# Kernel optimization log

Hardware: AMD Instinct MI355X
Metric: run time of the kernel (lower is better)

The kernel has to match this reference:

```python
import jax, jax.numpy as jnp
import numpy as np

B, C, H, W, N = 2, 128, 800, 640, 8192


def bilinear_sample(img, grid):
    """torch.F.grid_sample, mode='bilinear', padding_mode='border', align_corners=True.
    img: (B, C, H, W); grid: (B, P, 2) with (x, y) in [-1, 1]. Returns (B, C, P)."""
    _, _, h, w = img.shape
    x = jnp.clip((grid[..., 0] + 1.0) * 0.5 * (w - 1), 0.0, w - 1)  # border clip
    y = jnp.clip((grid[..., 1] + 1.0) * 0.5 * (h - 1), 0.0, h - 1)
    x0 = jnp.floor(x); y0 = jnp.floor(y)
    x0i = x0.astype(jnp.int32); y0i = y0.astype(jnp.int32)
    x1i = jnp.minimum(x0i + 1, w - 1); y1i = jnp.minimum(y0i + 1, h - 1)
    wx = (x - x0)[:, None, :]; wy = (y - y0)[:, None, :]
    g = jax.vmap(lambda im, yi, xi: im[:, yi, xi])  # per-batch gather -> (C, P)
    v00 = g(img, y0i, x0i); v01 = g(img, y0i, x1i)
    v10 = g(img, y1i, x0i); v11 = g(img, y1i, x1i)
    return (v00 * (1 - wx) * (1 - wy) + v01 * wx * (1 - wy)
            + v10 * (1 - wx) * wy + v11 * wx * wy)


def setup_inputs() -> dict:
    key = jax.random.key(0)
    ks = jax.random.split(key, 12)
    img = jax.random.normal(ks[0], (B, C, H, W), jnp.float32)
    verts = jax.random.uniform(ks[1], (B, N, 2), jnp.float32, minval=-1.0, maxval=1.0)
    # shift_delta Conv1d(C, 18, k=1) -- original inits to 0; use small random to exercise gathers
    W_sd = jax.random.normal(ks[2], (18, C), jnp.float32) * 0.01
    b_sd = jnp.zeros((18,), jnp.float32)
    s1 = 1.0 / np.sqrt(C + 2); s2 = 1.0 / np.sqrt(C)
    W_d1 = jax.random.normal(ks[3], (C, C + 2), jnp.float32) * s1
    b_d1 = jax.random.normal(ks[4], (C,), jnp.float32) * 0.01
    W_d2 = jax.random.normal(ks[5], (C, C), jnp.float32) * s2
    b_d2 = jax.random.normal(ks[6], (C,), jnp.float32) * 0.01
    # sum_neighbourhood Conv2d(C, C, kernel (1, 9)) -> weight (C, C, 9) after squeezing kh=1
    W_sn = jax.random.normal(ks[7], (C, C, 9), jnp.float32) * np.sqrt(2.0 / (C * 9))
    b_sn = jnp.zeros((C,), jnp.float32)
    W_c1 = jax.random.normal(ks[8], (C, C + 2), jnp.float32) * s1
    b_c1 = jax.random.normal(ks[9], (C,), jnp.float32) * 0.01
    W_c2 = jax.random.normal(ks[10], (C, C), jnp.float32) * s2
    b_c2 = jax.random.normal(ks[11], (C,), jnp.float32) * 0.01
    return dict(image_features=img, vertices=verts, W_sd=W_sd, b_sd=b_sd,
                W_d1=W_d1, b_d1=b_d1, W_d2=W_d2, b_d2=b_d2,
                W_sn=W_sn, b_sn=b_sn, W_c1=W_c1, b_c1=b_c1, W_c2=W_c2, b_c2=b_c2)


def reference(image_features, vertices, W_sd, b_sd, W_d1, b_d1, W_d2, b_d2,
              W_sn, b_sn, W_c1, b_c1, W_c2, b_c2):
    b, n, _ = vertices.shape
    c = image_features.shape[1]
    # sample at vertex centers: (B, C, N)
    feat_c = bilinear_sample(image_features, vertices)
    # Conv1d k=1 -> per-vertex linear producing 9 learned 2D offsets
    sd = (jnp.einsum('oc,bcn->bno', W_sd, feat_c) + b_sd).reshape(b, n, 9, 2)
    sd = sd.at[:, :, 0, :].set(0.0)  # offset 0 is the center itself
    nb = vertices[:, :, None, :] + sd                         # (B, N, 9, 2)
    f = bilinear_sample(image_features, nb.reshape(b, n * 9, 2)).reshape(b, c, n, 9)
    f = jnp.concatenate([f, nb.transpose(0, 3, 1, 2)], axis=1)  # (B, C+2, N, 9)
    d = f - f[:, :, :, :1]                                    # diff from center
    d = d.transpose(0, 3, 2, 1)                               # (B, 9, N, C+2)
    d = d @ W_d1.T + b_d1
    d = d @ W_d2.T + b_d2                                     # (B, 9, N, C)
    # Conv2d kernel (1, 9): contract neighbourhood axis -> (B, N, C)
    d = jnp.einsum('bknc,ock->bno', d, W_sn) + b_sn
    center = f[:, :, :, 0].transpose(0, 2, 1)                 # (B, N, C+2)
    center = (center @ W_c1.T + b_c1) @ W_c2.T + b_c2
    return center + d
```

## Files before the change

### kernel.cpp

```cpp
#include <hip/hip_runtime.h>
#include <cstdint>

#define BB 2
#define CC 128
#define IH 800
#define IW 640
#define NN 8192
#define HWp (IH * IW)
#define CE 130
#define WSL (CE * CC)
#define VPB 16

#define FADDR(e, v) (((e) << 4) + ((((e) >> 2)) << 2) + (v))
#define FSZ (FADDR(129, 15) + 1)


__device__ __forceinline__ void coords(float gx, float gy, int& xs, int& ys,
                                       float& ax, float& ay) {
  float x = (gx + 1.0f) * 0.5f * (float)(IW - 1);
  x = fminf(fmaxf(x, 0.0f), (float)(IW - 1));
  float y = (gy + 1.0f) * 0.5f * (float)(IH - 1);
  y = fminf(fmaxf(y, 0.0f), (float)(IH - 1));
  xs = min((int)x, IW - 2);
  ys = min((int)y, IH - 2);
  ax = x - (float)xs;
  ay = y - (float)ys;
}

struct GatIssue {
  float4 v0, v1;
  float ax, ay;
};

__device__ __forceinline__ GatIssue gat_issue(const float* __restrict__ imgT,
                                              int b, float gx, float gy, int l) {
  int xs, ys; float ax, ay;
  coords(gx, gy, xs, ys, ax, ay);
  const float* base = imgT + ((size_t)b * HWp + (size_t)ys * IW + xs) * CC;
  GatIssue g;
  g.v0 = *(const float4*)(base + l * 4);
  g.v1 = *(const float4*)(base + (size_t)IW * CC + l * 4);
  g.ax = ax; g.ay = ay;
  return g;
}

__device__ __forceinline__ float4 gat_finish(const GatIssue& g, int l) {
  float my = 1.0f - g.ay, mx = 1.0f - g.ax;
  float4 vy;
  vy.x = g.v0.x * my + g.v1.x * g.ay;
  vy.y = g.v0.y * my + g.v1.y * g.ay;
  vy.z = g.v0.z * my + g.v1.z * g.ay;
  vy.w = g.v0.w * my + g.v1.w * g.ay;
  float4 vo;
  vo.x = __shfl_xor(vy.x, 32, 64);
  vo.y = __shfl_xor(vy.y, 32, 64);
  vo.z = __shfl_xor(vy.z, 32, 64);
  vo.w = __shfl_xor(vy.w, 32, 64);
  float4 r;
  if (l < 32) {
    r.x = vy.x * mx + vo.x * g.ax;
    r.y = vy.y * mx + vo.y * g.ax;
    r.z = vy.z * mx + vo.z * g.ax;
    r.w = vy.w * mx + vo.w * g.ax;
  } else {
    r.x = vo.x * mx + vy.x * g.ax;
    r.y = vo.y * mx + vy.y * g.ax;
    r.z = vo.z * mx + vy.z * g.ax;
    r.w = vo.w * mx + vy.w * g.ax;
  }
  return r;
}

__device__ __forceinline__ float gat1_chw(const float* __restrict__ img, int b,
                                          int c, int xs, int ys, float ax, float ay) {
  const float* p = img + ((size_t)(b * CC + c) * IH + ys) * IW + xs;
  float v00 = p[0], v01 = p[1], v10 = p[IW], v11 = p[IW + 1];
  float my = 1.0f - ay, mx = 1.0f - ax;
  return (v00 * mx + v01 * ax) * my + (v10 * mx + v11 * ax) * ay;
}


__global__ void prep1(const float* __restrict__ W_d1, const float* __restrict__ b_d1,
                      const float* __restrict__ W_d2, const float* __restrict__ b_d2,
                      const float* __restrict__ W_c1, const float* __restrict__ b_c1,
                      const float* __restrict__ W_c2, const float* __restrict__ b_c2,
                      float* __restrict__ Wd, float* __restrict__ bdf,
                      float* __restrict__ Wcc, float* __restrict__ bcc) {
  int id = blockIdx.x;
  int e = threadIdx.x;
  if (id < 128) {
    int c = id;
    float acc = 0.0f;
    for (int c2 = 0; c2 < 128; ++c2)
      acc = fmaf(W_d2[c * 128 + c2], W_d1[c2 * CE + e], acc);
    Wd[c * CE + e] = acc;
    if (e == 0) {
      float bb = b_d2[c];
      for (int c2 = 0; c2 < 128; ++c2) bb = fmaf(W_d2[c * 128 + c2], b_d1[c2], bb);
      bdf[c] = bb;
    }
  } else {
    int o = id - 128;
    float acc = 0.0f;
    for (int c2 = 0; c2 < 128; ++c2)
      acc = fmaf(W_c2[o * 128 + c2], W_c1[c2 * CE + e], acc);
    Wcc[o * CE + e] = acc;
    if (e == 0) {
      float bb = b_c2[o];
      for (int c2 = 0; c2 < 128; ++c2) bb = fmaf(W_c2[o * 128 + c2], b_c1[c2], bb);
      bcc[o] = bb;
    }
  }
}

__global__ void prep2(const float* __restrict__ W_sn, const float* __restrict__ b_sn,
                      const float* __restrict__ Wd, const float* __restrict__ bdf,
                      const float* __restrict__ Wcc, const float* __restrict__ bcc,
                      float* __restrict__ Wcen, float* __restrict__ Wnb,
                      float* __restrict__ btot) {
  int eb = blockIdx.x;
  int o = threadIdx.x;
  float acc[9] = {0, 0, 0, 0, 0, 0, 0, 0, 0};
  float bacc = 0.0f;
  for (int c = 0; c < 128; ++c) {
    float wd = Wd[c * CE + eb];
    float bd = bdf[c];
    const float* sn = W_sn + (size_t)o * 1152 + c * 9;
    float ssum = 0.0f;
#pragma unroll
    for (int k = 0; k < 9; ++k) {
      float s = sn[k];
      acc[k] = fmaf(s, wd, acc[k]);
      ssum += s;
    }
    bacc = fmaf(ssum, bd, bacc);
  }
  float sum18 = 0.0f;
#pragma unroll
  for (int k = 1; k < 9; ++k) {
    Wnb[(size_t)(k - 1) * WSL + eb * 128 + o] = acc[k];
    sum18 += acc[k];
  }
  Wcen[eb * 128 + o] = Wcc[o * CE + eb] - sum18;
  if (eb == 0) btot[o] = bcc[o] + bacc + b_sn[o];
}


__global__ __launch_bounds__(256) void transpose_k(const float* __restrict__ img,
                                                   float* __restrict__ imgT) {
  __shared__ float tile[128][69];
  int b = blockIdx.y;
  size_t p0 = (size_t)blockIdx.x * 64;
  int t = threadIdx.x;
  int pq = t & 15, cr = t >> 4;
  float4 vr[8];
#pragma unroll
  for (int i = 0; i < 8; ++i) {
    int c = cr + (i << 4);
    vr[i] = *(const float4*)(img + (size_t)(b * CC + c) * HWp + p0 + pq * 4);
  }
#pragma unroll
  for (int i = 0; i < 8; ++i) {
    int c = cr + (i << 4);
    tile[c][pq * 4 + 0] = vr[i].x;
    tile[c][pq * 4 + 1] = vr[i].y;
    tile[c][pq * 4 + 2] = vr[i].z;
    tile[c][pq * 4 + 3] = vr[i].w;
  }
  __syncthreads();
  int c4 = (t & 31) << 2, pw = t >> 5;
#pragma unroll
  for (int i = 0; i < 8; ++i) {
    int p = pw + (i << 3);
    float4 v;
    v.x = tile[c4 + 0][p];
    v.y = tile[c4 + 1][p];
    v.z = tile[c4 + 2][p];
    v.w = tile[c4 + 3][p];
    *(float4*)(imgT + ((size_t)b * HWp + p0 + p) * CC + c4) = v;
  }
}


template <bool HWC>
__global__ __launch_bounds__(256) void fused_all(
    const float* __restrict__ imgp, const float* __restrict__ verts,
    const float* __restrict__ W_sd, const float* __restrict__ b_sd,
    const float* __restrict__ Wcen, const float* __restrict__ Wnb,
    const float* __restrict__ btot, float* __restrict__ out) {
  __shared__ __align__(16) float f[FSZ];
  __shared__ float sdl[VPB][18];
  __shared__ float nbc[VPB][16];
  __shared__ float red[128][17];
  int t = threadIdx.x;
  int o = t & 127, hs = t >> 7;
  int e0 = hs * 65;
  int v0 = blockIdx.x * VPB;
  int wv = t >> 6, l = t & 63;
  float acc[VPB] = {};

  if constexpr (HWC) {
    GatIssue g[4];
    float gxy[4][2];
#pragma unroll
    for (int s = 0; s < 4; ++s) {
      int vid = v0 + wv * 4 + s, b = vid >> 13;
      float gx = verts[vid * 2], gy = verts[vid * 2 + 1];
      gxy[s][0] = gx; gxy[s][1] = gy;
      g[s] = gat_issue(imgp, b, gx, gy, l);
    }
#pragma unroll
    for (int s = 0; s < 4; ++s) {
      int v = wv * 4 + s;
      float4 r = gat_finish(g[s], l);
      if (l < 32) {
        f[FADDR(4 * l + 0, v)] = r.x;
        f[FADDR(4 * l + 1, v)] = r.y;
        f[FADDR(4 * l + 2, v)] = r.z;
        f[FADDR(4 * l + 3, v)] = r.w;
      }
      if (l == 32) { f[FADDR(128, v)] = gxy[s][0]; f[FADDR(129, v)] = gxy[s][1]; }
    }
  } else {
    for (int s = 0; s < 4; ++s) {
      int v = wv * 4 + s, vid = v0 + v, b = vid >> 13;
      float gx = verts[vid * 2], gy = verts[vid * 2 + 1];
      int xs, ys; float ax, ay;
      coords(gx, gy, xs, ys, ax, ay);
      f[FADDR(l, v)] = gat1_chw(imgp, b, l, xs, ys, ax, ay);
      f[FADDR(l + 64, v)] = gat1_chw(imgp, b, l + 64, xs, ys, ax, ay);
      if (l == 0) { f[FADDR(128, v)] = gx; f[FADDR(129, v)] = gy; }
    }
  }
  __syncthreads();

  for (int idx = t; idx < VPB * 18; idx += 256) {
    int v = idx / 18, oo = idx - v * 18;
    float a = b_sd[oo];
    for (int c = 0; c < 128; ++c)
      a = fmaf(W_sd[oo * 128 + c], f[FADDR(c, v)], a);
    sdl[v][oo] = a;
  }

  {
    const float* Ws = Wcen;
    for (int e = e0; e < e0 + 65; ++e) {
      float w = Ws[e * 128 + o];
      const float4* fp = (const float4*)&f[FADDR(e, 0)];
      float4 fa = fp[0], fb = fp[1], fc = fp[2], fd = fp[3];
      acc[0]  = fmaf(fa.x, w, acc[0]);  acc[1]  = fmaf(fa.y, w, acc[1]);
      acc[2]  = fmaf(fa.z, w, acc[2]);  acc[3]  = fmaf(fa.w, w, acc[3]);
      acc[4]  = fmaf(fb.x, w, acc[4]);  acc[5]  = fmaf(fb.y, w, acc[5]);
      acc[6]  = fmaf(fb.z, w, acc[6]);  acc[7]  = fmaf(fb.w, w, acc[7]);
      acc[8]  = fmaf(fc.x, w, acc[8]);  acc[9]  = fmaf(fc.y, w, acc[9]);
      acc[10] = fmaf(fc.z, w, acc[10]); acc[11] = fmaf(fc.w, w, acc[11]);
      acc[12] = fmaf(fd.x, w, acc[12]); acc[13] = fmaf(fd.y, w, acc[13]);
      acc[14] = fmaf(fd.z, w, acc[14]); acc[15] = fmaf(fd.w, w, acc[15]);
    }
  }
  __syncthreads();

  {
    int v = t >> 4, j = t & 15, k = (j >> 1) + 1, comp = j & 1;
    int vid = v0 + v;
    nbc[v][j] = verts[vid * 2 + comp] + sdl[v][k * 2 + comp];
  }
  __syncthreads();

  for (int k = 0; k < 8; ++k) {
    if constexpr (HWC) {
      GatIssue g[4];
      float gxy[4][2];
#pragma unroll
      for (int s = 0; s < 4; ++s) {
        int v = wv * 4 + s, vid = v0 + v, b = vid >> 13;
        float gx = nbc[v][k * 2], gy = nbc[v][k * 2 + 1];
        gxy[s][0] = gx; gxy[s][1] = gy;
        g[s] = gat_issue(imgp, b, gx, gy, l);
      }
#pragma unroll
      for (int s = 0; s < 4; ++s) {
        int v = wv * 4 + s;
        float4 r = gat_finish(g[s], l);
        if (l < 32) {
          f[FADDR(4 * l + 0, v)] = r.x;
          f[FADDR(4 * l + 1, v)] = r.y;
          f[FADDR(4 * l + 2, v)] = r.z;
          f[FADDR(4 * l + 3, v)] = r.w;
        }
        if (l == 32) { f[FADDR(128, v)] = gxy[s][0]; f[FADDR(129, v)] = gxy[s][1]; }
      }
    } else {
      for (int s = 0; s < 4; ++s) {
        int v = wv * 4 + s, vid = v0 + v, b = vid >> 13;
        float gx = nbc[v][k * 2], gy = nbc[v][k * 2 + 1];
        int xs, ys; float ax, ay;
        coords(gx, gy, xs, ys, ax, ay);
        f[FADDR(l, v)] = gat1_chw(imgp, b, l, xs, ys, ax, ay);
        f[FADDR(l + 64, v)] = gat1_chw(imgp, b, l + 64, xs, ys, ax, ay);
        if (l == 0) { f[FADDR(128, v)] = gx; f[FADDR(129, v)] = gy; }
      }
    }
    __syncthreads();
    const float* Ws = Wnb + (size_t)k * WSL;
    for (int e = e0; e < e0 + 65; ++e) {
      float w = Ws[e * 128 + o];
      const float4* fp = (const float4*)&f[FADDR(e, 0)];
      float4 fa = fp[0], fb = fp[1], fc = fp[2], fd = fp[3];
      acc[0]  = fmaf(fa.x, w, acc[0]);  acc[1]  = fmaf(fa.y, w, acc[1]);
      acc[2]  = fmaf(fa.z, w, acc[2]);  acc[3]  = fmaf(fa.w, w, acc[3]);
      acc[4]  = fmaf(fb.x, w, acc[4]);  acc[5]  = fmaf(fb.y, w, acc[5]);
      acc[6]  = fmaf(fb.z, w, acc[6]);  acc[7]  = fmaf(fb.w, w, acc[7]);
      acc[8]  = fmaf(fc.x, w, acc[8]);  acc[9]  = fmaf(fc.y, w, acc[9]);
      acc[10] = fmaf(fc.z, w, acc[10]); acc[11] = fmaf(fc.w, w, acc[11]);
      acc[12] = fmaf(fd.x, w, acc[12]); acc[13] = fmaf(fd.y, w, acc[13]);
      acc[14] = fmaf(fd.z, w, acc[14]); acc[15] = fmaf(fd.w, w, acc[15]);
    }
    __syncthreads();
  }

  if (hs) {
#pragma unroll
    for (int j = 0; j < VPB; ++j) red[o][j] = acc[j];
  }
  __syncthreads();
  if (!hs) {
    float bt = btot[o];
#pragma unroll
    for (int j = 0; j < VPB; ++j)
      out[(size_t)(v0 + j) * CC + o] = acc[j] + red[o][j] + bt;
  }
}


extern "C" void kernel_launch(void* const* d_in, const int* in_sizes, int n_in,
                              void* d_out, int out_size, void* d_ws, size_t ws_size,
                              hipStream_t stream) {
  const float* img   = (const float*)d_in[0];
  const float* verts = (const float*)d_in[1];
  const float* W_sd  = (const float*)d_in[2];
  const float* b_sd  = (const float*)d_in[3];
  const float* W_d1  = (const float*)d_in[4];
  const float* b_d1  = (const float*)d_in[5];
  const float* W_d2  = (const float*)d_in[6];
  const float* b_d2  = (const float*)d_in[7];
  const float* W_sn  = (const float*)d_in[8];
  const float* b_sn  = (const float*)d_in[9];
  const float* W_c1  = (const float*)d_in[10];
  const float* b_c1  = (const float*)d_in[11];
  const float* W_c2  = (const float*)d_in[12];
  const float* b_c2  = (const float*)d_in[13];
  float* out = (float*)d_out;
  float* ws = (float*)d_ws;

  const size_t imgT_fl = (size_t)BB * HWp * CC;
  const size_t wt_fl   = 11 * (size_t)WSL + 384;
  bool hwc = ws_size >= (imgT_fl + wt_fl) * sizeof(float);

  float* base = ws;
  float* imgT = nullptr;
  if (hwc) { imgT = ws; base = ws + imgT_fl; }
  float* Wd   = base;  base += WSL;
  float* bdf  = base;  base += 128;
  float* Wcc  = base;  base += WSL;
  float* bcc  = base;  base += 128;
  float* Wcen = base;  base += WSL;
  float* Wnb  = base;  base += 8 * WSL;
  float* btot = base;

  if (hwc) transpose_k<<<dim3(HWp / 64, BB), 256, 0, stream>>>(img, imgT);
  prep1<<<256, 130, 0, stream>>>(W_d1, b_d1, W_d2, b_d2, W_c1, b_c1, W_c2, b_c2,
                                 Wd, bdf, Wcc, bcc);
  prep2<<<130, 128, 0, stream>>>(W_sn, b_sn, Wd, bdf, Wcc, bcc, Wcen, Wnb, btot);

  if (hwc) {
    fused_all<true><<<BB * NN / VPB, 256, 0, stream>>>(imgT, verts, W_sd, b_sd,
                                                       Wcen, Wnb, btot, out);
  } else {
    fused_all<false><<<BB * NN / VPB, 256, 0, stream>>>(img, verts, W_sd, b_sd,
                                                        Wcen, Wnb, btot, out);
  }
}
```

Baseline: 1.027 ms.

## Store transposed image in fp16, precompute shift projection, and double-buffer gathers

The image transpose now writes a half-precision HWC copy. The same pass also computes the 18-channel shift-delta projection for every pixel, so per-vertex offsets come from a bilinear sample of that projection rather than a per-block 128-wide dot product. The fused kernel double-buffers the feature tile so the next neighbour's gathers are issued while the current slice's GEMM runs, and each thread now covers two output channels and 8 vertices. The intent is to cut transpose and gather traffic and hide gather latency, at the cost of fp16 rounding of image features and an extra full-image projection write.

Measured after the change: 1.971 ms. 1.92x slower.

```diff
diff --git a/kernel.cpp b/kernel.cpp
--- a/kernel.cpp
+++ b/kernel.cpp
@@ -1,4 +1,5 @@
 #include <hip/hip_runtime.h>
+#include <hip/hip_fp16.h>
 #include <cstdint>
 
 #define BB 2
@@ -27,48 +28,49 @@
   ay = y - (float)ys;
 }
 
-struct GatIssue {
-  float4 v0, v1;
+struct GatH {
+  uint4 q;
   float ax, ay;
 };
 
-__device__ __forceinline__ GatIssue gat_issue(const float* __restrict__ imgT,
-                                              int b, float gx, float gy, int l) {
+__device__ __forceinline__ GatH gath_issue(const __half* __restrict__ imgT,
+                                           int b, float gx, float gy, int l) {
   int xs, ys; float ax, ay;
   coords(gx, gy, xs, ys, ax, ay);
-  const float* base = imgT + ((size_t)b * HWp + (size_t)ys * IW + xs) * CC;
-  GatIssue g;
-  g.v0 = *(const float4*)(base + l * 4);
-  g.v1 = *(const float4*)(base + (size_t)IW * CC + l * 4);
+  const __half* base = imgT + ((size_t)b * HWp + (size_t)ys * IW + xs) * CC;
+  const __half* row = base + ((l >= 32) ? (size_t)IW * CC : 0);
+  GatH g;
+  g.q = *(const uint4*)(row + (l & 31) * 8);
   g.ax = ax; g.ay = ay;
   return g;
 }
 
-__device__ __forceinline__ float4 gat_finish(const GatIssue& g, int l) {
+__device__ __forceinline__ void gath_finish_store(const GatH& g, int l,
+                                                  float* __restrict__ f, int v,
+                                                  float gx, float gy) {
+  float m8[8];
+  const __half2* h2 = (const __half2*)&g.q;
+#pragma unroll
+  for (int w = 0; w < 4; ++w) {
+    float2 f2 = __half22float2(h2[w]);
+    m8[2 * w] = f2.x; m8[2 * w + 1] = f2.y;
+  }
   float my = 1.0f - g.ay, mx = 1.0f - g.ax;
-  float4 vy;
-  vy.x = g.v0.x * my + g.v1.x * g.ay;
-  vy.y = g.v0.y * my + g.v1.y * g.ay;
-  vy.z = g.v0.z * my + g.v1.z * g.ay;
-  vy.w = g.v0.w * my + g.v1.w * g.ay;
-  float4 vo;
-  vo.x = __shfl_xor(vy.x, 32, 64);
-  vo.y = __shfl_xor(vy.y, 32, 64);
-  vo.z = __shfl_xor(vy.z, 32, 64);
-  vo.w = __shfl_xor(vy.w, 32, 64);
-  float4 r;
+  float r8[8];
+#pragma unroll
+  for (int j = 0; j < 8; ++j) {
+    float oth = __shfl_xor(m8[j], 32);
+    float rv = (l < 32) ? (m8[j] * my + oth * g.ay) : (oth * my + m8[j] * g.ay);
+    float ox = __shfl_xor(rv, 16);
+    r8[j] = (l & 16) ? (ox * mx + rv * g.ax) : (rv * mx + ox * g.ax);
+  }
   if (l < 32) {
-    r.x = vy.x * mx + vo.x * g.ax;
-    r.y = vy.y * mx + vo.y * g.ax;
-    r.z = vy.z * mx + vo.z * g.ax;
-    r.w = vy.w * mx + vo.w * g.ax;
-  } else {
-    r.x = vo.x * mx + vy.x * g.ax;
-    r.y = vo.y * mx + vy.y * g.ax;
-    r.z = vo.z * mx + vy.z * g.ax;
-    r.w = vo.w * mx + vy.w * g.ax;
-  }
-  return r;
+    int m = l & 15;
+    int jb = (l & 16) ? 4 : 0;
+#pragma unroll
+    for (int j = 0; j < 4; ++j) f[FADDR(8 * m + jb + j, v)] = r8[jb + j];
+  }
+  if (l == 32) { f[FADDR(128, v)] = gx; f[FADDR(129, v)] = gy; }
 }
 
 __device__ __forceinline__ float gat1_chw(const float* __restrict__ img, int b,
@@ -146,12 +148,15 @@
 }
 
 
-__global__ __launch_bounds__(256) void transpose_k(const float* __restrict__ img,
-                                                   float* __restrict__ imgT) {
+__global__ __launch_bounds__(256) void prep_img(const float* __restrict__ img,
+                                                const float* __restrict__ W_sd,
+                                                __half* __restrict__ imgT,
+                                                float* __restrict__ sdimg) {
   __shared__ float tile[128][69];
   int b = blockIdx.y;
   size_t p0 = (size_t)blockIdx.x * 64;
   int t = threadIdx.x;
+
   int pq = t & 15, cr = t >> 4;
   float4 vr[8];
 #pragma unroll
@@ -168,23 +173,146 @@
     tile[c][pq * 4 + 3] = vr[i].w;
   }
   __syncthreads();
-  int c4 = (t & 31) << 2, pw = t >> 5;
-#pragma unroll
-  for (int i = 0; i < 8; ++i) {
-    int p = pw + (i << 3);
-    float4 v;
-    v.x = tile[c4 + 0][p];
-    v.y = tile[c4 + 1][p];
-    v.z = tile[c4 + 2][p];
-    v.w = tile[c4 + 3][p];
-    *(float4*)(imgT + ((size_t)b * HWp + p0 + p) * CC + c4) = v;
-  }
-}
-
-
-template <bool HWC>
-__global__ __launch_bounds__(256) void fused_all(
-    const float* __restrict__ imgp, const float* __restrict__ verts,
+
+  int c8 = (t & 15) * 8, pw0 = t >> 4;
+#pragma unroll
+  for (int r = 0; r < 4; ++r) {
+    int p = pw0 + (r << 4);
+    uint4 q;
+    __half2* h2 = (__half2*)&q;
+#pragma unroll
+    for (int w = 0; w < 4; ++w)
+      h2[w] = __floats2half2_rn(tile[c8 + 2 * w][p], tile[c8 + 2 * w + 1][p]);
+    *(uint4*)(imgT + ((size_t)b * HWp + p0 + p) * CC + c8) = q;
+  }
+
+  int px = t & 63;
+  int jg = __builtin_amdgcn_readfirstlane(t >> 6);
+  int jbase = (jg < 2) ? jg * 5 : 10 + (jg - 2) * 4;
+  int jn = (jg < 2) ? 5 : 4;
+  float acc[5] = {0, 0, 0, 0, 0};
+  for (int c = 0; c < 128; ++c) {
+    float v = tile[c][px];
+    for (int m = 0; m < jn; ++m)
+      acc[m] = fmaf(W_sd[(jbase + m) * 128 + c], v, acc[m]);
+  }
+  for (int m = 0; m < jn; ++m)
+    sdimg[((size_t)b * HWp + p0 + px) * 18 + jbase + m] = acc[m];
+}
+
+
+__device__ __forceinline__ void gemm_slice(const float* __restrict__ fb,
+                                           const float* __restrict__ Ws,
+                                           int l, int eb, int vbase,
+                                           float acc0[8], float acc1[8]) {
+  for (int e = eb; e < eb + 65; ++e) {
+    float w0 = Ws[e * 128 + l];
+    float w1 = Ws[e * 128 + 64 + l];
+    const float4* fp = (const float4*)&fb[FADDR(e, vbase)];
+    float4 fa = fp[0], fb4 = fp[1];
+    acc0[0] = fmaf(fa.x, w0, acc0[0]);  acc1[0] = fmaf(fa.x, w1, acc1[0]);
+    acc0[1] = fmaf(fa.y, w0, acc0[1]);  acc1[1] = fmaf(fa.y, w1, acc1[1]);
+    acc0[2] = fmaf(fa.z, w0, acc0[2]);  acc1[2] = fmaf(fa.z, w1, acc1[2]);
+    acc0[3] = fmaf(fa.w, w0, acc0[3]);  acc1[3] = fmaf(fa.w, w1, acc1[3]);
+    acc0[4] = fmaf(fb4.x, w0, acc0[4]); acc1[4] = fmaf(fb4.x, w1, acc1[4]);
+    acc0[5] = fmaf(fb4.y, w0, acc0[5]); acc1[5] = fmaf(fb4.y, w1, acc1[5]);
+    acc0[6] = fmaf(fb4.z, w0, acc0[6]); acc1[6] = fmaf(fb4.z, w1, acc1[6]);
+    acc0[7] = fmaf(fb4.w, w0, acc0[7]); acc1[7] = fmaf(fb4.w, w1, acc1[7]);
+  }
+}
+
+__global__ __launch_bounds__(256) void fused_hwc(
+    const __half* __restrict__ imgT, const float* __restrict__ sdimg,
+    const float* __restrict__ verts, const float* __restrict__ b_sd,
+    const float* __restrict__ Wcen, const float* __restrict__ Wnb,
+    const float* __restrict__ btot, float* __restrict__ out) {
+  __shared__ __align__(16) float f0[FSZ], f1[FSZ];
+  __shared__ float sdl[VPB][18];
+  __shared__ float nbc[VPB][16];
+  __shared__ float red[128][17];
+  int t = threadIdx.x;
+  int v0 = blockIdx.x * VPB;
+  int wv = t >> 6, l = t & 63;
+  int vg = (t >> 6) & 1, hs = t >> 7;
+  int eb = hs * 65, vbase = vg * 8;
+  float acc0[8] = {}, acc1[8] = {};
+
+  GatH g[4]; float gxy[4][2];
+#pragma unroll
+  for (int s = 0; s < 4; ++s) {
+    int vid = v0 + wv * 4 + s;
+    float gx = verts[vid * 2], gy = verts[vid * 2 + 1];
+    gxy[s][0] = gx; gxy[s][1] = gy;
+    g[s] = gath_issue(imgT, vid >> 13, gx, gy, l);
+  }
+
+  for (int idx = t; idx < VPB * 18; idx += 256) {
+    int v = idx / 18, j = idx - v * 18;
+    int vid = v0 + v, b = vid >> 13;
+    float gx = verts[vid * 2], gy = verts[vid * 2 + 1];
+    int xs, ys; float ax, ay;
+    coords(gx, gy, xs, ys, ax, ay);
+    const float* sp = sdimg + ((size_t)b * HWp + (size_t)ys * IW + xs) * 18 + j;
+    float v00 = sp[0], v01 = sp[18];
+    float v10 = sp[(size_t)IW * 18], v11 = sp[(size_t)IW * 18 + 18];
+    float my = 1.0f - ay, mx = 1.0f - ax;
+    sdl[v][j] = (v00 * mx + v01 * ax) * my + (v10 * mx + v11 * ax) * ay + b_sd[j];
+  }
+  __syncthreads();
+  {
+    int v = t >> 4, j2 = t & 15;
+    int vid = v0 + v;
+    nbc[v][j2] = verts[vid * 2 + (j2 & 1)] + sdl[v][2 + j2];
+  }
+#pragma unroll
+  for (int s = 0; s < 4; ++s)
+    gath_finish_store(g[s], l, f0, wv * 4 + s, gxy[s][0], gxy[s][1]);
+  __syncthreads();
+
+  const float* fb = f0;
+  for (int s = 0; s < 9; ++s) {
+    float* fnext = (s & 1) ? f0 : f1;
+    if (s < 8) {
+#pragma unroll
+      for (int q = 0; q < 4; ++q) {
+        int v = wv * 4 + q, vid = v0 + v;
+        float gx = nbc[v][2 * s], gy = nbc[v][2 * s + 1];
+        gxy[q][0] = gx; gxy[q][1] = gy;
+        g[q] = gath_issue(imgT, vid >> 13, gx, gy, l);
+      }
+    }
+    const float* Ws = (s == 0) ? Wcen : Wnb + (size_t)(s - 1) * WSL;
+    gemm_slice(fb, Ws, l, eb, vbase, acc0, acc1);
+    if (s < 8) {
+#pragma unroll
+      for (int q = 0; q < 4; ++q)
+        gath_finish_store(g[q], l, fnext, wv * 4 + q, gxy[q][0], gxy[q][1]);
+    }
+    __syncthreads();
+    fb = fnext;
+  }
+
+  if (hs) {
+#pragma unroll
+    for (int j = 0; j < 8; ++j) {
+      red[l][vbase + j] = acc0[j];
+      red[l + 64][vbase + j] = acc1[j];
+    }
+  }
+  __syncthreads();
+  if (!hs) {
+    float b0 = btot[l], b1 = btot[l + 64];
+#pragma unroll
+    for (int j = 0; j < 8; ++j) {
+      out[(size_t)(v0 + vbase + j) * CC + l]      = acc0[j] + red[l][vbase + j] + b0;
+      out[(size_t)(v0 + vbase + j) * CC + l + 64] = acc1[j] + red[l + 64][vbase + j] + b1;
+    }
+  }
+}
+
+
+__global__ __launch_bounds__(256) void fused_chw(
+    const float* __restrict__ img, const float* __restrict__ verts,
     const float* __restrict__ W_sd, const float* __restrict__ b_sd,
     const float* __restrict__ Wcen, const float* __restrict__ Wnb,
     const float* __restrict__ btot, float* __restrict__ out) {
@@ -199,38 +327,14 @@
   int wv = t >> 6, l = t & 63;
   float acc[VPB] = {};
 
-  if constexpr (HWC) {
-    GatIssue g[4];
-    float gxy[4][2];
-#pragma unroll
-    for (int s = 0; s < 4; ++s) {
-      int vid = v0 + wv * 4 + s, b = vid >> 13;
-      float gx = verts[vid * 2], gy = verts[vid * 2 + 1];
-      gxy[s][0] = gx; gxy[s][1] = gy;
-      g[s] = gat_issue(imgp, b, gx, gy, l);
-    }
-#pragma unroll
-    for (int s = 0; s < 4; ++s) {
-      int v = wv * 4 + s;
-      float4 r = gat_finish(g[s], l);
-      if (l < 32) {
-        f[FADDR(4 * l + 0, v)] = r.x;
-        f[FADDR(4 * l + 1, v)] = r.y;
-        f[FADDR(4 * l + 2, v)] = r.z;
-        f[FADDR(4 * l + 3, v)] = r.w;
-      }
-      if (l == 32) { f[FADDR(128, v)] = gxy[s][0]; f[FADDR(129, v)] = gxy[s][1]; }
-    }
-  } else {
-    for (int s = 0; s < 4; ++s) {
-      int v = wv * 4 + s, vid = v0 + v, b = vid >> 13;
-      float gx = verts[vid * 2], gy = verts[vid * 2 + 1];
-      int xs, ys; float ax, ay;
-      coords(gx, gy, xs, ys, ax, ay);
-      f[FADDR(l, v)] = gat1_chw(imgp, b, l, xs, ys, ax, ay);
-      f[FADDR(l + 64, v)] = gat1_chw(imgp, b, l + 64, xs, ys, ax, ay);
-      if (l == 0) { f[FADDR(128, v)] = gx; f[FADDR(129, v)] = gy; }
-    }
+  for (int s = 0; s < 4; ++s) {
+    int v = wv * 4 + s, vid = v0 + v, b = vid >> 13;
+    float gx = verts[vid * 2], gy = verts[vid * 2 + 1];
+    int xs, ys; float ax, ay;
+    coords(gx, gy, xs, ys, ax, ay);
+    f[FADDR(l, v)] = gat1_chw(img, b, l, xs, ys, ax, ay);
+    f[FADDR(l + 64, v)] = gat1_chw(img, b, l + 64, xs, ys, ax, ay);
+    if (l == 0) { f[FADDR(128, v)] = gx; f[FADDR(129, v)] = gy; }
   }
   __syncthreads();
 
@@ -259,7 +363,6 @@
     }
   }
   __syncthreads();
-
   {
     int v = t >> 4, j = t & 15, k = (j >> 1) + 1, comp = j & 1;
     int vid = v0 + v;
@@ -268,38 +371,14 @@
   __syncthreads();
 
   for (int k = 0; k < 8; ++k) {
-    if constexpr (HWC) {
-      GatIssue g[4];
-      float gxy[4][2];
-#pragma unroll
-      for (int s = 0; s < 4; ++s) {
-        int v = wv * 4 + s, vid = v0 + v, b = vid >> 13;
-        float gx = nbc[v][k * 2], gy = nbc[v][k * 2 + 1];
-        gxy[s][0] = gx; gxy[s][1] = gy;
-        g[s] = gat_issue(imgp, b, gx, gy, l);
-      }
-#pragma unroll
-      for (int s = 0; s < 4; ++s) {
-        int v = wv * 4 + s;
-        float4 r = gat_finish(g[s], l);
-        if (l < 32) {
-          f[FADDR(4 * l + 0, v)] = r.x;
-          f[FADDR(4 * l + 1, v)] = r.y;
-          f[FADDR(4 * l + 2, v)] = r.z;
-          f[FADDR(4 * l + 3, v)] = r.w;
-        }
-        if (l == 32) { f[FADDR(128, v)] = gxy[s][0]; f[FADDR(129, v)] = gxy[s][1]; }
-      }
-    } else {
-      for (int s = 0; s < 4; ++s) {
-        int v = wv * 4 + s, vid = v0 + v, b = vid >> 13;
-        float gx = nbc[v][k * 2], gy = nbc[v][k * 2 + 1];
-        int xs, ys; float ax, ay;
-        coords(gx, gy, xs, ys, ax, ay);
-        f[FADDR(l, v)] = gat1_chw(imgp, b, l, xs, ys, ax, ay);
-        f[FADDR(l + 64, v)] = gat1_chw(imgp, b, l + 64, xs, ys, ax, ay);
-        if (l == 0) { f[FADDR(128, v)] = gx; f[FADDR(129, v)] = gy; }
-      }
+    for (int s = 0; s < 4; ++s) {
+      int v = wv * 4 + s, vid = v0 + v, b = vid >> 13;
+      float gx = nbc[v][k * 2], gy = nbc[v][k * 2 + 1];
+      int xs, ys; float ax, ay;
+      coords(gx, gy, xs, ys, ax, ay);
+      f[FADDR(l, v)] = gat1_chw(img, b, l, xs, ys, ax, ay);
+      f[FADDR(l + 64, v)] = gat1_chw(img, b, l + 64, xs, ys, ax, ay);
+      if (l == 0) { f[FADDR(128, v)] = gx; f[FADDR(129, v)] = gy; }
     }
     __syncthreads();
     const float* Ws = Wnb + (size_t)k * WSL;
@@ -321,14 +400,14 @@
 
   if (hs) {
 #pragma unroll
-    for (int j = 0; j < VPB; ++j) red[o][j] = acc[j];
+    for (int j = 0; j < VPB; ++j) red[o][j & 15] = acc[j];
   }
   __syncthreads();
   if (!hs) {
     float bt = btot[o];
 #pragma unroll
     for (int j = 0; j < VPB; ++j)
-      out[(size_t)(v0 + j) * CC + o] = acc[j] + red[o][j] + bt;
+      out[(size_t)(v0 + j) * CC + o] = acc[j] + red[o][j & 15] + bt;
   }
 }
 
@@ -351,33 +430,39 @@
   const float* W_c2  = (const float*)d_in[12];
   const float* b_c2  = (const float*)d_in[13];
   float* out = (float*)d_out;
-  float* ws = (float*)d_ws;
-
-  const size_t imgT_fl = (size_t)BB * HWp * CC;
-  const size_t wt_fl   = 11 * (size_t)WSL + 384;
-  bool hwc = ws_size >= (imgT_fl + wt_fl) * sizeof(float);
-
-  float* base = ws;
-  float* imgT = nullptr;
-  if (hwc) { imgT = ws; base = ws + imgT_fl; }
-  float* Wd   = base;  base += WSL;
-  float* bdf  = base;  base += 128;
-  float* Wcc  = base;  base += WSL;
-  float* bcc  = base;  base += 128;
-  float* Wcen = base;  base += WSL;
-  float* Wnb  = base;  base += 8 * WSL;
-  float* btot = base;
-
-  if (hwc) transpose_k<<<dim3(HWp / 64, BB), 256, 0, stream>>>(img, imgT);
+
+  const size_t imgT_bytes = (size_t)BB * HWp * CC * 2;
+  const size_t sdimg_fl   = (size_t)BB * HWp * 18;
+  const size_t wt_fl      = 11 * (size_t)WSL + 384;
+  bool hwc = ws_size >= imgT_bytes + (sdimg_fl + wt_fl) * sizeof(float);
+
+  char* base = (char*)d_ws;
+  __half* imgT = nullptr;
+  float* sdimg = nullptr;
+  if (hwc) {
+    imgT = (__half*)base;
+    sdimg = (float*)(base + imgT_bytes);
+    base = (char*)(sdimg + sdimg_fl);
+  }
+  float* fbase = (float*)base;
+  float* Wd   = fbase;  fbase += WSL;
+  float* bdf  = fbase;  fbase += 128;
+  float* Wcc  = fbase;  fbase += WSL;
+  float* bcc  = fbase;  fbase += 128;
+  float* Wcen = fbase;  fbase += WSL;
+  float* Wnb  = fbase;  fbase += 8 * WSL;
+  float* btot = fbase;
+
   prep1<<<256, 130, 0, stream>>>(W_d1, b_d1, W_d2, b_d2, W_c1, b_c1, W_c2, b_c2,
                                  Wd, bdf, Wcc, bcc);
   prep2<<<130, 128, 0, stream>>>(W_sn, b_sn, Wd, bdf, Wcc, bcc, Wcen, Wnb, btot);
 
   if (hwc) {
-    fused_all<true><<<BB * NN / VPB, 256, 0, stream>>>(imgT, verts, W_sd, b_sd,
-                                                       Wcen, Wnb, btot, out);
+    prep_img<<<dim3(HWp / 64, BB), 256, 0, stream>>>(img, W_sd, imgT, sdimg);
+    fused_hwc<<<BB * NN / VPB, 256, 0, stream>>>(imgT, sdimg, verts, b_sd,
+                                                 Wcen, Wnb, btot, out);
   } else {
-    fused_all<false><<<BB * NN / VPB, 256, 0, stream>>>(img, verts, W_sd, b_sd,
-                                                        Wcen, Wnb, btot, out);
-  }
-}
+    fused_chw<<<BB * NN / VPB, 256, 0, stream>>>(img, verts, W_sd, b_sd,
+                                                 Wcen, Wnb, btot, out);
+  }
+}
```
